# Optimization experiments

Measured on AMD Instinct MI355X. Metric: run time of the kernel, lower is better.

Reference implementation:

```python
import jax, jax.numpy as jnp
from jax import lax
import numpy as np

B, T, S, U, E, V = 64, 50, 50, 1024, 100, 30001


def setup_inputs() -> dict:
    key = jax.random.key(0)
    ks = jax.random.split(key, 12)
    sc = 0.02
    return {
        "tokens": jax.random.randint(ks[0], (B, T), 0, V, dtype=jnp.int32),
        "memory": jax.random.normal(ks[1], (B, S, U), jnp.float32),
        "h0": jax.random.normal(ks[2], (B, U), jnp.float32),
        "c0": jax.random.normal(ks[3], (B, U), jnp.float32),
        "emb": jax.random.normal(ks[4], (V, E), jnp.float32) * sc,
        "Wx": jax.random.normal(ks[5], (E + U, 4 * U), jnp.float32) * sc,
        "Uh": jax.random.normal(ks[6], (U, 4 * U), jnp.float32) * sc,
        "b": jnp.zeros((4 * U,), jnp.float32),
        "Wm": jax.random.normal(ks[7], (U, U), jnp.float32) * sc,
        "Wa": jax.random.normal(ks[8], (2 * U, U), jnp.float32) * sc,
        "Wo": jax.random.normal(ks[9], (U, V), jnp.float32) * sc,
        "bo": jnp.zeros((V,), jnp.float32),
    }


def reference(tokens, memory, h0, c0, emb, Wx, Uh, b, Wm, Wa, Wo, bo):
    # Luong memory layer: keys = memory @ Wm (Dense(units, use_bias=False))
    keys = jnp.einsum("bsu,uk->bsk", memory, Wm)  # [B,S,U]
    x_emb = emb[tokens]                            # [B,T,E] teacher-forced inputs

    def step(carry, x_t):
        h, c, attn = carry
        # AttentionWrapper cell input: concat(embedding, prev attention)
        z = jnp.concatenate([x_t, attn], axis=-1) @ Wx + h @ Uh + b  # [B,4U]
        i, f, g, o = jnp.split(z, 4, axis=-1)  # keras gate order i,f,c,o
        c_new = jax.nn.sigmoid(f) * c + jax.nn.sigmoid(i) * jnp.tanh(g)
        h_new = jax.nn.sigmoid(o) * jnp.tanh(c_new)
        # Luong score: query (h_new) dot processed memory keys
        score = jnp.einsum("bu,bsu->bs", h_new, keys)
        align = jax.nn.softmax(score, axis=-1)
        ctx = jnp.einsum("bs,bsu->bu", align, memory)
        # attention_layer: Dense(units, use_bias=False) on concat(cell_out, ctx)
        attn_new = jnp.concatenate([h_new, ctx], axis=-1) @ Wa
        logits = attn_new @ Wo + bo  # output_layer
        return (h_new, c_new, attn_new), logits

    init = (h0, c0, jnp.zeros_like(h0))
    _, logits = lax.scan(step, init, jnp.swapaxes(x_emb, 0, 1))  # [T,B,V]
    return jnp.transpose(logits, (1, 0, 2))  # [B,T,V]
```

## Files before the change

### kernel.cpp

```cpp
#include <hip/hip_runtime.h>
#include <math.h>

#define B_  64
#define T_  50
#define S_  50
#define U_  1024
#define E_  100
#define V_  30001
#define U4_ 4096
#define VP_ 30080
#define HCSTR_ 131136

typedef __bf16 bf16_t;
typedef bf16_t bf16x8 __attribute__((ext_vector_type(8)));
typedef float  f32x4  __attribute__((ext_vector_type(4)));
typedef unsigned long long u64_t;

__device__ __forceinline__ float2 scload8(const float* p) {
    u64_t v = __hip_atomic_load((const u64_t*)p, __ATOMIC_RELAXED,
                                __HIP_MEMORY_SCOPE_SYSTEM);
    union { u64_t u; float2 f; } c; c.u = v; return c.f;
}
__device__ __forceinline__ void scstore8(float* p, float x, float y) {
    union { u64_t u; float2 f; } c; c.f = make_float2(x, y);
    __hip_atomic_store((u64_t*)p, c.u, __ATOMIC_RELAXED,
                       __HIP_MEMORY_SCOPE_SYSTEM);
}
__device__ __forceinline__ unsigned scload_u(const unsigned* p) {
    return __hip_atomic_load(p, __ATOMIC_RELAXED, __HIP_MEMORY_SCOPE_SYSTEM);
}
__device__ __forceinline__ void scadd_u(unsigned* p) {
    __hip_atomic_fetch_add(p, 1u, __ATOMIC_RELAXED, __HIP_MEMORY_SCOPE_SYSTEM);
}
__device__ __forceinline__ void vm_drain() {
    asm volatile("s_waitcnt vmcnt(0)" ::: "memory");
}
__device__ __forceinline__ void cbar() { asm volatile("" ::: "memory"); }

__global__ void add_inplace(float* __restrict__ dst, const float* __restrict__ src, int n)
{
    int i = blockIdx.x * blockDim.x + threadIdx.x;
    if (i < n) dst[i] += src[i];
}

__global__ void gather_emb_pad(const int* __restrict__ tokens,
                               const float* __restrict__ emb,
                               float* __restrict__ xe)
{
    const int r = blockIdx.x;
    const int e = threadIdx.x;
    float v;
    if (e < E_)       v = emb[(size_t)tokens[r] * E_ + e];
    else if (e == E_) v = 1.f;
    else              v = 0.f;
    xe[(size_t)r * 128 + e] = v;
}

__global__ void pad_wx(const float* __restrict__ Wx,
                       const float* __restrict__ bvec,
                       float* __restrict__ dst)
{
    const int col = blockIdx.x * 256 + threadIdx.x;
    const int row = blockIdx.y;
    float v;
    if (row < E_)       v = Wx[(size_t)row * U4_ + col];
    else if (row == E_) v = bvec[col];
    else                v = 0.f;
    dst[(size_t)row * U4_ + col] = v;
}

__global__ __launch_bounds__(256) void transpose_wo(
    const float* __restrict__ wo, bf16_t* __restrict__ dst)
{
    __shared__ bf16_t tile[64][72];
    const int c0 = blockIdx.x * 64;
    const int k0 = blockIdx.y * 64;
    const int tx = threadIdx.x & 63, ty = threadIdx.x >> 6;

#pragma unroll
    for (int kk = ty; kk < 64; kk += 4) {
        const int col = c0 + tx;
        float v = (col < V_) ? wo[(size_t)(k0 + kk) * V_ + col] : 0.f;
        tile[kk][tx] = (bf16_t)v;
    }
    __syncthreads();
#pragma unroll
    for (int cc = ty; cc < 64; cc += 4)
        dst[(size_t)(c0 + cc) * 1024 + k0 + tx] = tile[tx][cc];
}

template <int OUT>
__global__ __launch_bounds__(256) void gemm_mfma_split(
    const float* __restrict__ A, int lda,
    const float* __restrict__ Bm, int ldb,
    float* __restrict__ C, int ldc, int K)
{
    __shared__ bf16_t As_h[128][40];
    __shared__ bf16_t As_l[128][40];
    __shared__ bf16_t Bs_h[128][40];
    __shared__ bf16_t Bs_l[128][40];

    const int n0  = blockIdx.x * 128;
    const int m0  = blockIdx.y * 128;
    const int tid = threadIdx.x;
    const int wave = tid >> 6, lane = tid & 63;
    const int wr = wave >> 1, wc = wave & 1;
    const int lr = lane & 15;
    const int lk = lane >> 4;

    f32x4 acc[4][4] = {};

    const int ar  = tid >> 1, ak = (tid & 1) * 16;
    const int bk0 = (tid >> 5) * 4, bc = (tid & 31) * 4;

    for (int k0 = 0; k0 < K; k0 += 32) {
        {
            const float* ap = &A[(size_t)(m0 + ar) * lda + k0 + ak];
            bf16x8 h0v, l0v, h1v, l1v;
#pragma unroll
            for (int q = 0; q < 2; ++q) {
                float4 v0 = *(const float4*)&ap[q * 8];
                float4 v1 = *(const float4*)&ap[q * 8 + 4];
                float xs[8] = {v0.x, v0.y, v0.z, v0.w, v1.x, v1.y, v1.z, v1.w};
#pragma unroll
                for (int e = 0; e < 8; ++e) {
                    bf16_t h = (bf16_t)xs[e];
                    if (q == 0) { h0v[e] = h; l0v[e] = (bf16_t)(xs[e] - (float)h); }
                    else        { h1v[e] = h; l1v[e] = (bf16_t)(xs[e] - (float)h); }
                }
            }
            *(bf16x8*)&As_h[ar][ak]     = h0v;
            *(bf16x8*)&As_h[ar][ak + 8] = h1v;
            *(bf16x8*)&As_l[ar][ak]     = l0v;
            *(bf16x8*)&As_l[ar][ak + 8] = l1v;
        }
        {
#pragma unroll
            for (int kk = 0; kk < 4; ++kk) {
                float4 v = *(const float4*)&Bm[(size_t)(k0 + bk0 + kk) * ldb + n0 + bc];
                float xs[4] = {v.x, v.y, v.z, v.w};
#pragma unroll
                for (int i = 0; i < 4; ++i) {
                    bf16_t h = (bf16_t)xs[i];
                    Bs_h[bc + i][bk0 + kk] = h;
                    Bs_l[bc + i][bk0 + kk] = (bf16_t)(xs[i] - (float)h);
                }
            }
        }
        __syncthreads();

        bf16x8 ah[4], alv[4], bh[4], bl[4];
#pragma unroll
        for (int m = 0; m < 4; ++m) {
            ah[m]  = *(const bf16x8*)&As_h[wr * 64 + m * 16 + lr][lk * 8];
            alv[m] = *(const bf16x8*)&As_l[wr * 64 + m * 16 + lr][lk * 8];
        }
#pragma unroll
        for (int n = 0; n < 4; ++n) {
            bh[n] = *(const bf16x8*)&Bs_h[wc * 64 + n * 16 + lr][lk * 8];
            bl[n] = *(const bf16x8*)&Bs_l[wc * 64 + n * 16 + lr][lk * 8];
        }
#pragma unroll
        for (int m = 0; m < 4; ++m)
#pragma unroll
            for (int n = 0; n < 4; ++n) {
                acc[m][n] = __builtin_amdgcn_mfma_f32_16x16x32_bf16(ah[m],  bh[n], acc[m][n], 0, 0, 0);
                acc[m][n] = __builtin_amdgcn_mfma_f32_16x16x32_bf16(ah[m],  bl[n], acc[m][n], 0, 0, 0);
                acc[m][n] = __builtin_amdgcn_mfma_f32_16x16x32_bf16(alv[m], bh[n], acc[m][n], 0, 0, 0);
            }
        __syncthreads();
    }

#pragma unroll
    for (int m = 0; m < 4; ++m) {
        const int row = m0 + wr * 64 + m * 16 + lk * 4;
#pragma unroll
        for (int n = 0; n < 4; ++n) {
            const int col = n0 + wc * 64 + n * 16 + lr;
#pragma unroll
            for (int r = 0; r < 4; ++r) {
                if (OUT == 0)
                    C[(size_t)(row + r) * ldc + col] = acc[m][n][r];
                else
                    ((bf16_t*)C)[(size_t)(row + r) * ldc + col] = (bf16_t)acc[m][n][r];
            }
        }
    }
}

__global__ __launch_bounds__(256) void zgemm_partial(
    const float* __restrict__ A, int lda,
    const float* __restrict__ Bm,
    float* __restrict__ zp)
{
    __shared__ float As[64][17];
    __shared__ float Bs[16][68];

    const int n0     = blockIdx.x * 64;
    const int ks     = blockIdx.y;
    const int k_base = ks * 256;
    const int tid    = threadIdx.x;
    const int tx     = tid & 15, ty = tid >> 4;

    float acc[4][4];
#pragma unroll
    for (int i = 0; i < 4; ++i)
#pragma unroll
        for (int j = 0; j < 4; ++j) acc[i][j] = 0.f;

    const int ra = tid >> 2, ca = (tid & 3) * 4;
    const int rb = tid >> 4, cb = (tid & 15) * 4;

    for (int kt = 0; kt < 16; ++kt) {
        const int k0 = k_base + kt * 16;
        float4 av = *(const float4*)&A[(size_t)ra * lda + k0 + ca];
        As[ra][ca + 0] = av.x;
        As[ra][ca + 1] = av.y;
        As[ra][ca + 2] = av.z;
        As[ra][ca + 3] = av.w;
        float4 bv = *(const float4*)&Bm[(size_t)(k0 + rb) * U4_ + n0 + cb];
        *(float4*)&Bs[rb][cb] = bv;
        __syncthreads();
#pragma unroll
        for (int kk = 0; kk < 16; ++kk) {
            float a_[4];
#pragma unroll
            for (int i = 0; i < 4; ++i) a_[i] = As[ty * 4 + i][kk];
            float4 bq = *(const float4*)&Bs[kk][tx * 4];
            float b_[4] = {bq.x, bq.y, bq.z, bq.w};
#pragma unroll
            for (int i = 0; i < 4; ++i)
#pragma unroll
                for (int j = 0; j < 4; ++j)
                    acc[i][j] = fmaf(a_[i], b_[j], acc[i][j]);
        }
        __syncthreads();
    }

#pragma unroll
    for (int i = 0; i < 4; ++i)
        *(float4*)&zp[((size_t)ks * 64 + ty * 4 + i) * U4_ + n0 + tx * 4] =
            make_float4(acc[i][0], acc[i][1], acc[i][2], acc[i][3]);
}

__global__ __launch_bounds__(512) void decoder_loop12(
    const float* __restrict__ zemb,
    const float* __restrict__ Wcomb,
    const float* __restrict__ keys,
    const float* __restrict__ memory,
    const float* __restrict__ c0,
    float* __restrict__ hcbuf,
    float* __restrict__ zp,
    float* __restrict__ hc_all,
    unsigned* flags)
{
    static __shared__ __attribute__((aligned(16))) char smem[153088];
    bf16_t* wfr = (bf16_t*)smem;
    float*  tr  = (float*)(smem + 131072);
    float*  hs  = (float*)(smem + 148480);
    float*  sc  = (float*)(smem + 152576);
    float*  al  = (float*)(smem + 152832);

    const int beta = blockIdx.x;
    const int tid  = threadIdx.x;

    const int nt = beta & 63, ks = beta >> 6;
    const int koff = ks * 512;
    const int c0c  = nt * 64;

    for (int i = tid; i < 512 * 64; i += 512) {
        const int k = i >> 6, col = i & 63;
        const float w = Wcomb[(size_t)(koff + k) * U4_ + c0c + col];
        const bf16_t hi = (bf16_t)w;
        const bf16_t lo = (bf16_t)(w - (float)hi);
        const int ntile = col >> 4, lane_lo = col & 15;
        const int kk = k >> 5, kr = k & 31;
        const int lane = (kr >> 3) * 16 + lane_lo, j = kr & 7;
        const int base = ((ntile * 16 + kk) * 2) * 512 + lane * 8 + j;
        wfr[base]       = hi;
        wfr[base + 512] = lo;
    }

    const int b  = beta;
    const int u2 = tid * 2;
    float creg[2] = {0.f, 0.f};
    if (beta < 64) {
        float2 cv = *(const float2*)&c0[b * U_ + u2];
        creg[0] = cv.x;
        creg[1] = cv.y;
    }
    __syncthreads();

    const int w  = tid >> 6, l = tid & 63;
    const int mt = w >> 1, ntb = (w & 1) * 2;
    const int arow = mt * 16 + (l & 15);
    const int aq   = l >> 4;
    const size_t abase = (size_t)arow * 2048 + koff + aq * 8;

    for (int t = 0; t < T_; ++t) {
        if (t) {
            {
                const unsigned tgt = 8u * (unsigned)t;
                const unsigned* fb = (ks < 2) ? &flags[512] : &flags[768];
                if (tid < 8) {
                    const unsigned* f = fb + tid * 32;
                    while (scload_u(f) < tgt) __builtin_amdgcn_s_sleep(1);
                }
                __syncthreads();
                cbar();
            }

            const float* ap = &hcbuf[(size_t)(t - 1) * HCSTR_ + abase];

            float4 a0[16], a1[16];
#pragma unroll
            for (int kk = 0; kk < 16; ++kk) {
                a0[kk] = *(const float4*)&ap[kk * 32];
                a1[kk] = *(const float4*)&ap[kk * 32 + 4];
            }

            f32x4 acc[2] = {};
#pragma unroll
            for (int kk = 0; kk < 16; ++kk) {
                float xs[8] = {a0[kk].x, a0[kk].y, a0[kk].z, a0[kk].w,
                               a1[kk].x, a1[kk].y, a1[kk].z, a1[kk].w};
                bf16x8 ah, alv;
#pragma unroll
                for (int e = 0; e < 8; ++e) {
                    bf16_t h = (bf16_t)xs[e];
                    ah[e]  = h;
                    alv[e] = (bf16_t)(xs[e] - (float)h);
                }
#pragma unroll
                for (int nn = 0; nn < 2; ++nn) {
                    const int fb2 = (((ntb + nn) * 16 + kk) * 2) * 512 + l * 8;
                    bf16x8 bh = *(const bf16x8*)&wfr[fb2];
                    bf16x8 bl = *(const bf16x8*)&wfr[fb2 + 512];
                    acc[nn] = __builtin_amdgcn_mfma_f32_16x16x32_bf16(ah, bh, acc[nn], 0, 0, 0);
                    acc[nn] = __builtin_amdgcn_mfma_f32_16x16x32_bf16(ah, bl, acc[nn], 0, 0, 0);
                    acc[nn] = __builtin_amdgcn_mfma_f32_16x16x32_bf16(alv, bh, acc[nn], 0, 0, 0);
                }
            }

#pragma unroll
            for (int nn = 0; nn < 2; ++nn)
#pragma unroll
                for (int rr = 0; rr < 4; ++rr)
                    tr[(mt * 16 + (l >> 4) * 4 + rr) * 68 + (ntb + nn) * 16 + (l & 15)] =
                        acc[nn][rr];
            __syncthreads();

            {
                const int zb = tid >> 3, cg = (tid & 7) * 8;
                float4 r0 = *(const float4*)&tr[zb * 68 + cg];
                float4 r1 = *(const float4*)&tr[zb * 68 + cg + 4];
                float* zrow = &zp[((size_t)(ks * 64 + zb)) * U4_ + c0c + cg];
                scstore8(zrow + 0, r0.x, r0.y);
                scstore8(zrow + 2, r0.z, r0.w);
                scstore8(zrow + 4, r1.x, r1.y);
                scstore8(zrow + 6, r1.z, r1.w);
            }
            vm_drain();
            __syncthreads();
            if (tid == 0) scadd_u(&flags[(beta & 15) * 32]);
        }

        if (beta < 64) {
            if (t) {
                const unsigned tgt = 16u * (unsigned)t;
                if (tid < 16) {
                    const unsigned* f = &flags[tid * 32];
                    while (scload_u(f) < tgt) __builtin_amdgcn_s_sleep(1);
                }
                __syncthreads();
                cbar();
            }

            const float* ze = &zemb[((size_t)b * T_ + t) * U4_];
            float zgx[4], zgy[4];
#pragma unroll
            for (int g = 0; g < 4; ++g) {
                float2 a = *(const float2*)&ze[g * U_ + u2];
                zgx[g] = a.x;
                zgy[g] = a.y;
            }
#pragma unroll
            for (int s = 0; s < 4; ++s) {
#pragma unroll
                for (int g = 0; g < 4; ++g) {
                    float2 v = scload8(&zp[((size_t)s * 64 + b) * U4_ + g * U_ + u2]);
                    zgx[g] += v.x;
                    zgy[g] += v.y;
                }
            }

            const float six = 1.f / (1.f + expf(-zgx[0]));
            const float sfx = 1.f / (1.f + expf(-zgx[1]));
            const float tgx = tanhf(zgx[2]);
            const float sox = 1.f / (1.f + expf(-zgx[3]));
            const float cnx = sfx * creg[0] + six * tgx;
            creg[0] = cnx;
            const float hnx = sox * tanhf(cnx);

            const float siy = 1.f / (1.f + expf(-zgy[0]));
            const float sfy = 1.f / (1.f + expf(-zgy[1]));
            const float tgy = tanhf(zgy[2]);
            const float soy = 1.f / (1.f + expf(-zgy[3]));
            const float cny = sfy * creg[1] + siy * tgy;
            creg[1] = cny;
            const float hny = soy * tanhf(cny);

            float* hcb_t = &hcbuf[(size_t)t * HCSTR_];
            hs[u2]     = hnx;
            hs[u2 + 1] = hny;
            scstore8(&hcb_t[b * 2048 + u2], hnx, hny);
            *(float2*)&hc_all[((size_t)b * T_ + t) * 2048 + u2] =
                make_float2(hnx, hny);
            vm_drain();
            __syncthreads();
            if (tid == 0) scadd_u(&flags[512 + (b & 7) * 32]);

            const int lane = tid & 63, wv = tid >> 6;
            for (int s = wv; s < S_; s += 8) {
                const float* kp = &keys[((size_t)b * S_ + s) * U_ + lane * 16];
                const float* hp = &hs[lane * 16];
                float p = 0.f;
#pragma unroll
                for (int q = 0; q < 4; ++q) {
                    float4 kv = *(const float4*)&kp[q * 4];
                    float4 hv = *(const float4*)&hp[q * 4];
                    p = fmaf(hv.x, kv.x, p);
                    p = fmaf(hv.y, kv.y, p);
                    p = fmaf(hv.z, kv.z, p);
                    p = fmaf(hv.w, kv.w, p);
                }
#pragma unroll
                for (int off = 32; off > 0; off >>= 1)
                    p += __shfl_xor(p, off);
                if (lane == 0) sc[s] = p;
            }
            __syncthreads();

            if (tid < 64) {
                float v = (tid < S_) ? sc[tid] : -INFINITY;
                float m = v;
#pragma unroll
                for (int off = 32; off > 0; off >>= 1)
                    m = fmaxf(m, __shfl_xor(m, off));
                float e = (tid < S_) ? expf(v - m) : 0.f;
                float ssum = e;
#pragma unroll
                for (int off = 32; off > 0; off >>= 1)
                    ssum += __shfl_xor(ssum, off);
                if (tid < S_) al[tid] = e / ssum;
            }
            __syncthreads();

            {
                const float2* mp = (const float2*)&memory[(size_t)b * S_ * U_];
                float cx = 0.f, cy = 0.f;
#pragma unroll 10
                for (int s = 0; s < S_; ++s) {
                    float2 mv = mp[s * 512 + tid];
                    const float a = al[s];
                    cx = fmaf(a, mv.x, cx);
                    cy = fmaf(a, mv.y, cy);
                }
                scstore8(&hcb_t[b * 2048 + U_ + u2], cx, cy);
                *(float2*)&hc_all[((size_t)b * T_ + t) * 2048 + U_ + u2] =
                    make_float2(cx, cy);
            }
            vm_drain();
            __syncthreads();
            if (tid == 0) scadd_u(&flags[768 + (b & 7) * 32]);
        }
    }
}

__global__ __launch_bounds__(256) void gemm_wo_mfma3(
    const bf16_t* __restrict__ A,
    const bf16_t* __restrict__ Bt,
    const float*  __restrict__ bias,
    float* __restrict__ C)
{
    __shared__ bf16_t As[2][128][40];
    __shared__ bf16_t Bs[2][128][40];

    const int n0  = blockIdx.x * 128;
    const int m0  = blockIdx.y * 128;
    const int tid = threadIdx.x;
    const int wave = tid >> 6, lane = tid & 63;
    const int wr = wave >> 1, wc = wave & 1;
    const int lr = lane & 15;
    const int lk = lane >> 4;

    f32x4 acc[4][4] = {};

    const int ar = tid >> 1, ak = (tid & 1) * 16;
    const bf16_t* apb = &A[(size_t)(m0 + ar) * U_ + ak];
    const bf16_t* bpb = &Bt[(size_t)(n0 + ar) * U_ + ak];

    {
        *(bf16x8*)&As[0][ar][ak]     = *(const bf16x8*)&apb[0];
        *(bf16x8*)&As[0][ar][ak + 8] = *(const bf16x8*)&apb[8];
        *(bf16x8*)&Bs[0][ar][ak]     = *(const bf16x8*)&bpb[0];
        *(bf16x8*)&Bs[0][ar][ak + 8] = *(const bf16x8*)&bpb[8];
    }
    __syncthreads();

    for (int k0 = 0; k0 < U_; k0 += 32) {
        const int cur = (k0 >> 5) & 1;
        bf16x8 na0, na1, nb0, nb1;
        const bool more = (k0 + 32 < U_);
        if (more) {
            na0 = *(const bf16x8*)&apb[k0 + 32];
            na1 = *(const bf16x8*)&apb[k0 + 40];
            nb0 = *(const bf16x8*)&bpb[k0 + 32];
            nb1 = *(const bf16x8*)&bpb[k0 + 40];
        }

        bf16x8 af[4], bf[4];
#pragma unroll
        for (int m = 0; m < 4; ++m)
            af[m] = *(const bf16x8*)&As[cur][wr * 64 + m * 16 + lr][lk * 8];
#pragma unroll
        for (int n = 0; n < 4; ++n)
            bf[n] = *(const bf16x8*)&Bs[cur][wc * 64 + n * 16 + lr][lk * 8];
#pragma unroll
        for (int m = 0; m < 4; ++m)
#pragma unroll
            for (int n = 0; n < 4; ++n)
                acc[m][n] = __builtin_amdgcn_mfma_f32_16x16x32_bf16(
                    af[m], bf[n], acc[m][n], 0, 0, 0);

        if (more) {
            *(bf16x8*)&As[cur ^ 1][ar][ak]     = na0;
            *(bf16x8*)&As[cur ^ 1][ar][ak + 8] = na1;
            *(bf16x8*)&Bs[cur ^ 1][ar][ak]     = nb0;
            *(bf16x8*)&Bs[cur ^ 1][ar][ak + 8] = nb1;
        }
        __syncthreads();
    }

#pragma unroll
    for (int m = 0; m < 4; ++m) {
        const int row = m0 + wr * 64 + m * 16 + lk * 4;
#pragma unroll
        for (int n = 0; n < 4; ++n) {
            const int col = n0 + wc * 64 + n * 16 + lr;
            if (col < V_) {
                const float bb = bias[col];
#pragma unroll
                for (int r = 0; r < 4; ++r)
                    C[(size_t)(row + r) * V_ + col] = acc[m][n][r] + bb;
            }
        }
    }
}

extern "C" void kernel_launch(void* const* d_in, const int* in_sizes, int n_in,
                              void* d_out, int out_size, void* d_ws, size_t ws_size,
                              hipStream_t stream)
{
    const int*   tokens = (const int*)  d_in[0];
    const float* memory = (const float*)d_in[1];
    const float* h0     = (const float*)d_in[2];
    const float* c0     = (const float*)d_in[3];
    const float* emb    = (const float*)d_in[4];
    const float* Wx     = (const float*)d_in[5];
    const float* Uh     = (const float*)d_in[6];
    const float* bvec   = (const float*)d_in[7];
    const float* Wm     = (const float*)d_in[8];
    const float* Wa     = (const float*)d_in[9];
    const float* Wo     = (const float*)d_in[10];
    const float* bo     = (const float*)d_in[11];
    float* out = (float*)d_out;

    float* ws = (float*)d_ws;
    size_t off = 0;
    float*   Wcomb  = ws + off; off += (size_t)2048 * U4_;
    float*   keys   = ws + off; off += (size_t)B_ * S_ * U_;
    float*   hc_all = ws + off; off += (size_t)B_ * T_ * 2048;
    float*   zp     = ws + off; off += (size_t)4 * B_ * U4_;
    float*   x_emb  = ws + off; off += (size_t)B_ * T_ * 128;
    unsigned* flags = (unsigned*)(ws + off); off += 1024;
    bf16_t*  wo_t   = (bf16_t*)(ws + off); off += (size_t)VP_ * 1024 / 2;

    float* zemb   = out;
    float* hcbuf  = out + (size_t)3200 * U4_;
    float* wx_pad = out + (size_t)3200 * U4_ + (size_t)T_ * HCSTR_;
    bf16_t* abf   = (bf16_t*)Wcomb;

    (void)ws_size;
    (void)hipMemsetAsync(flags, 0, 1024 * sizeof(unsigned), stream);

    gather_emb_pad<<<B_ * T_, 128, 0, stream>>>(tokens, emb, x_emb);
    pad_wx<<<dim3(U4_ / 256, 128), 256, 0, stream>>>(Wx, bvec, wx_pad);
    gemm_mfma_split<0><<<dim3(32, 25), 256, 0, stream>>>(
        x_emb, 128, wx_pad, U4_, zemb, U4_, 128);
    gemm_mfma_split<0><<<dim3(32, 16), 256, 0, stream>>>(
        Wa, U_, Wx + (size_t)E_ * U4_, U4_, Wcomb, U4_, U_);
    add_inplace<<<(1024 * U4_) / 256, 256, 0, stream>>>(Wcomb, Uh, 1024 * U4_);
    gemm_mfma_split<0><<<dim3(8, 25), 256, 0, stream>>>(
        memory, U_, Wm, U_, keys, U_, U_);
    zgemm_partial<<<dim3(64, 4), 256, 0, stream>>>(h0, U_, Uh, zp);
    transpose_wo<<<dim3(VP_ / 64, 1024 / 64), 256, 0, stream>>>(Wo, wo_t);

    decoder_loop12<<<256, 512, 0, stream>>>(
        zemb, Wcomb, keys, memory, c0, hcbuf, zp, hc_all, flags);

    gemm_mfma_split<1><<<dim3(8, 25), 256, 0, stream>>>(
        hc_all, 2048, Wa, U_, (float*)abf, U_, 2048);
    gemm_wo_mfma3<<<dim3(VP_ / 128, 25), 256, 0, stream>>>(abf, wo_t, bo, out);
}
```

Before: 2.147 ms.

## Precompute memory projected through the ctx rows of Wcomb to halve the recurrent GEMM K

Precomputes M2 = memory @ Wcomb[ctx rows] ahead of the loop. The context term of the gates then becomes an alignment-weighted sum over M2 inside the owning block, so the recurrent MFMA GEMM only needs h (K=1024 instead of 2048). This removes the context flag wait and the cross-block context exchange, and halves each block's LDS weight slice. The per-step context vectors for the output path are rebuilt afterwards by a separate ctx_recon kernel from the stored alignments. In exchange there is an extra large precompute GEMM, and each step streams 50x4096 floats of M2 per batch row, which is more global traffic on the serial critical path.

Result: slower. 2.672 ms (+24.4%).

```diff
diff --git a/kernel.cpp b/kernel.cpp
--- a/kernel.cpp
+++ b/kernel.cpp
@@ -9,22 +9,22 @@
 #define V_  30001
 #define U4_ 4096
 #define VP_ 30080
-#define HCSTR_ 131136
+#define HSTR_ 65600
 
 typedef __bf16 bf16_t;
 typedef bf16_t bf16x8 __attribute__((ext_vector_type(8)));
 typedef float  f32x4  __attribute__((ext_vector_type(4)));
 typedef unsigned long long u64_t;
 
+__device__ __forceinline__ void scstore8(float* p, float x, float y) {
+    union { u64_t u; float2 f; } c; c.f = make_float2(x, y);
+    __hip_atomic_store((u64_t*)p, c.u, __ATOMIC_RELAXED,
+                       __HIP_MEMORY_SCOPE_SYSTEM);
+}
 __device__ __forceinline__ float2 scload8(const float* p) {
     u64_t v = __hip_atomic_load((const u64_t*)p, __ATOMIC_RELAXED,
                                 __HIP_MEMORY_SCOPE_SYSTEM);
     union { u64_t u; float2 f; } c; c.u = v; return c.f;
-}
-__device__ __forceinline__ void scstore8(float* p, float x, float y) {
-    union { u64_t u; float2 f; } c; c.f = make_float2(x, y);
-    __hip_atomic_store((u64_t*)p, c.u, __ATOMIC_RELAXED,
-                       __HIP_MEMORY_SCOPE_SYSTEM);
 }
 __device__ __forceinline__ unsigned scload_u(const unsigned* p) {
     return __hip_atomic_load(p, __ATOMIC_RELAXED, __HIP_MEMORY_SCOPE_SYSTEM);
@@ -243,32 +243,65 @@
             make_float4(acc[i][0], acc[i][1], acc[i][2], acc[i][3]);
 }
 
-__global__ __launch_bounds__(512) void decoder_loop12(
+__global__ __launch_bounds__(512) void ctx_recon(
+    const float* __restrict__ align_all,
+    const float* __restrict__ memory,
+    float* __restrict__ hc_all)
+{
+    __shared__ float alds[T_ * 64];
+    const int b = blockIdx.x, tid = threadIdx.x;
+    for (int i = tid; i < T_ * 64; i += 512)
+        alds[i] = align_all[(size_t)b * T_ * 64 + i];
+    __syncthreads();
+    const int u2 = tid * 2;
+    for (int t0 = 0; t0 < T_; t0 += 10) {
+        float ax[10], ay[10];
+#pragma unroll
+        for (int q = 0; q < 10; ++q) { ax[q] = 0.f; ay[q] = 0.f; }
+        for (int s = 0; s < S_; ++s) {
+            float2 mv = *(const float2*)&memory[((size_t)b * S_ + s) * U_ + u2];
+#pragma unroll
+            for (int q = 0; q < 10; ++q) {
+                float a = alds[(t0 + q) * 64 + s];
+                ax[q] = fmaf(a, mv.x, ax[q]);
+                ay[q] = fmaf(a, mv.y, ay[q]);
+            }
+        }
+#pragma unroll
+        for (int q = 0; q < 10; ++q)
+            *(float2*)&hc_all[((size_t)b * T_ + t0 + q) * 2048 + U_ + u2] =
+                make_float2(ax[q], ay[q]);
+    }
+}
+
+__global__ __launch_bounds__(512) void decoder_loop13(
     const float* __restrict__ zemb,
     const float* __restrict__ Wcomb,
+    const float* __restrict__ M2,
     const float* __restrict__ keys,
     const float* __restrict__ memory,
     const float* __restrict__ c0,
-    float* __restrict__ hcbuf,
+    float* __restrict__ hbuf,
     float* __restrict__ zp,
     float* __restrict__ hc_all,
+    float* __restrict__ align_all,
     unsigned* flags)
 {
-    static __shared__ __attribute__((aligned(16))) char smem[153088];
+    static __shared__ __attribute__((aligned(16))) char smem[87552];
     bf16_t* wfr = (bf16_t*)smem;
-    float*  tr  = (float*)(smem + 131072);
-    float*  hs  = (float*)(smem + 148480);
-    float*  sc  = (float*)(smem + 152576);
-    float*  al  = (float*)(smem + 152832);
+    float*  tr  = (float*)(smem + 65536);
+    float*  hs  = (float*)(smem + 82944);
+    float*  sc  = (float*)(smem + 87040);
+    float*  al  = (float*)(smem + 87296);
 
     const int beta = blockIdx.x;
     const int tid  = threadIdx.x;
 
     const int nt = beta & 63, ks = beta >> 6;
-    const int koff = ks * 512;
+    const int koff = ks * 256;
     const int c0c  = nt * 64;
 
-    for (int i = tid; i < 512 * 64; i += 512) {
+    for (int i = tid; i < 256 * 64; i += 512) {
         const int k = i >> 6, col = i & 63;
         const float w = Wcomb[(size_t)(koff + k) * U4_ + c0c + col];
         const bf16_t hi = (bf16_t)w;
@@ -276,7 +309,7 @@
         const int ntile = col >> 4, lane_lo = col & 15;
         const int kk = k >> 5, kr = k & 31;
         const int lane = (kr >> 3) * 16 + lane_lo, j = kr & 7;
-        const int base = ((ntile * 16 + kk) * 2) * 512 + lane * 8 + j;
+        const int base = ((ntile * 8 + kk) * 2) * 512 + lane * 8 + j;
         wfr[base]       = hi;
         wfr[base + 512] = lo;
     }
@@ -284,6 +317,8 @@
     const int b  = beta;
     const int u2 = tid * 2;
     float creg[2] = {0.f, 0.f};
+    float zalx[4] = {0.f, 0.f, 0.f, 0.f};
+    float zaly[4] = {0.f, 0.f, 0.f, 0.f};
     if (beta < 64) {
         float2 cv = *(const float2*)&c0[b * U_ + u2];
         creg[0] = cv.x;
@@ -295,35 +330,28 @@
     const int mt = w >> 1, ntb = (w & 1) * 2;
     const int arow = mt * 16 + (l & 15);
     const int aq   = l >> 4;
-    const size_t abase = (size_t)arow * 2048 + koff + aq * 8;
+    const size_t abase = (size_t)arow * U_ + koff + aq * 8;
 
     for (int t = 0; t < T_; ++t) {
         if (t) {
             {
                 const unsigned tgt = 8u * (unsigned)t;
-                const unsigned* fb = (ks < 2) ? &flags[512] : &flags[768];
                 if (tid < 8) {
-                    const unsigned* f = fb + tid * 32;
+                    const unsigned* f = &flags[512 + tid * 32];
                     while (scload_u(f) < tgt) __builtin_amdgcn_s_sleep(1);
                 }
                 __syncthreads();
                 cbar();
             }
 
-            const float* ap = &hcbuf[(size_t)(t - 1) * HCSTR_ + abase];
-
-            float4 a0[16], a1[16];
-#pragma unroll
-            for (int kk = 0; kk < 16; ++kk) {
-                a0[kk] = *(const float4*)&ap[kk * 32];
-                a1[kk] = *(const float4*)&ap[kk * 32 + 4];
-            }
+            const float* ap = &hbuf[(size_t)(t - 1) * HSTR_ + abase];
 
             f32x4 acc[2] = {};
 #pragma unroll
-            for (int kk = 0; kk < 16; ++kk) {
-                float xs[8] = {a0[kk].x, a0[kk].y, a0[kk].z, a0[kk].w,
-                               a1[kk].x, a1[kk].y, a1[kk].z, a1[kk].w};
+            for (int kk = 0; kk < 8; ++kk) {
+                float4 a0 = *(const float4*)&ap[kk * 32];
+                float4 a1 = *(const float4*)&ap[kk * 32 + 4];
+                float xs[8] = {a0.x, a0.y, a0.z, a0.w, a1.x, a1.y, a1.z, a1.w};
                 bf16x8 ah, alv;
 #pragma unroll
                 for (int e = 0; e < 8; ++e) {
@@ -333,7 +361,7 @@
                 }
 #pragma unroll
                 for (int nn = 0; nn < 2; ++nn) {
-                    const int fb2 = (((ntb + nn) * 16 + kk) * 2) * 512 + l * 8;
+                    const int fb2 = (((ntb + nn) * 8 + kk) * 2) * 512 + l * 8;
                     bf16x8 bh = *(const bf16x8*)&wfr[fb2];
                     bf16x8 bl = *(const bf16x8*)&wfr[fb2 + 512];
                     acc[nn] = __builtin_amdgcn_mfma_f32_16x16x32_bf16(ah, bh, acc[nn], 0, 0, 0);
@@ -381,8 +409,8 @@
 #pragma unroll
             for (int g = 0; g < 4; ++g) {
                 float2 a = *(const float2*)&ze[g * U_ + u2];
-                zgx[g] = a.x;
-                zgy[g] = a.y;
+                zgx[g] = a.x + zalx[g];
+                zgy[g] = a.y + zaly[g];
             }
 #pragma unroll
             for (int s = 0; s < 4; ++s) {
@@ -410,10 +438,9 @@
             creg[1] = cny;
             const float hny = soy * tanhf(cny);
 
-            float* hcb_t = &hcbuf[(size_t)t * HCSTR_];
             hs[u2]     = hnx;
             hs[u2 + 1] = hny;
-            scstore8(&hcb_t[b * 2048 + u2], hnx, hny);
+            scstore8(&hbuf[(size_t)t * HSTR_ + b * U_ + u2], hnx, hny);
             *(float2*)&hc_all[((size_t)b * T_ + t) * 2048 + u2] =
                 make_float2(hnx, hny);
             vm_drain();
@@ -452,27 +479,26 @@
 #pragma unroll
                 for (int off = 32; off > 0; off >>= 1)
                     ssum += __shfl_xor(ssum, off);
-                if (tid < S_) al[tid] = e / ssum;
+                al[tid] = (tid < S_) ? e / ssum : 0.f;
             }
             __syncthreads();
 
-            {
-                const float2* mp = (const float2*)&memory[(size_t)b * S_ * U_];
-                float cx = 0.f, cy = 0.f;
-#pragma unroll 10
-                for (int s = 0; s < S_; ++s) {
-                    float2 mv = mp[s * 512 + tid];
-                    const float a = al[s];
-                    cx = fmaf(a, mv.x, cx);
-                    cy = fmaf(a, mv.y, cy);
-                }
-                scstore8(&hcb_t[b * 2048 + U_ + u2], cx, cy);
-                *(float2*)&hc_all[((size_t)b * T_ + t) * 2048 + U_ + u2] =
-                    make_float2(cx, cy);
-            }
-            vm_drain();
-            __syncthreads();
-            if (tid == 0) scadd_u(&flags[768 + (b & 7) * 32]);
+            if (tid < 64)
+                align_all[((size_t)b * T_ + t) * 64 + tid] = al[tid];
+
+#pragma unroll
+            for (int g = 0; g < 4; ++g) { zalx[g] = 0.f; zaly[g] = 0.f; }
+            const float* m2b = &M2[(size_t)b * S_ * U4_];
+            for (int s = 0; s < S_; ++s) {
+                const float a = al[s];
+                const float* mr = &m2b[(size_t)s * U4_];
+#pragma unroll
+                for (int g = 0; g < 4; ++g) {
+                    float2 mv = *(const float2*)&mr[g * U_ + u2];
+                    zalx[g] = fmaf(a, mv.x, zalx[g]);
+                    zaly[g] = fmaf(a, mv.y, zaly[g]);
+                }
+            }
         }
     }
 }
@@ -578,18 +604,20 @@
 
     float* ws = (float*)d_ws;
     size_t off = 0;
-    float*   Wcomb  = ws + off; off += (size_t)2048 * U4_;
-    float*   keys   = ws + off; off += (size_t)B_ * S_ * U_;
-    float*   hc_all = ws + off; off += (size_t)B_ * T_ * 2048;
-    float*   zp     = ws + off; off += (size_t)4 * B_ * U4_;
-    float*   x_emb  = ws + off; off += (size_t)B_ * T_ * 128;
-    unsigned* flags = (unsigned*)(ws + off); off += 1024;
-    bf16_t*  wo_t   = (bf16_t*)(ws + off); off += (size_t)VP_ * 1024 / 2;
+    float*   keys    = ws + off; off += (size_t)B_ * S_ * U_;
+    float*   hc_all  = ws + off; off += (size_t)B_ * T_ * 2048;
+    float*   zp      = ws + off; off += (size_t)4 * B_ * U4_;
+    float*   x_emb   = ws + off; off += (size_t)B_ * T_ * 128;
+    float*   al_all  = ws + off; off += (size_t)B_ * T_ * 64;
+    unsigned* flags  = (unsigned*)(ws + off); off += 1024;
+    bf16_t*  wo_t    = (bf16_t*)(ws + off); off += (size_t)VP_ * 1024 / 2;
 
     float* zemb   = out;
-    float* hcbuf  = out + (size_t)3200 * U4_;
-    float* wx_pad = out + (size_t)3200 * U4_ + (size_t)T_ * HCSTR_;
-    bf16_t* abf   = (bf16_t*)Wcomb;
+    float* hbuf   = zemb + (size_t)3200 * U4_;
+    float* wx_pad = hbuf + (size_t)T_ * HSTR_;
+    float* Wcomb  = wx_pad + (size_t)128 * U4_;
+    float* M2     = Wcomb + (size_t)2048 * U4_;
+    bf16_t* abf   = (bf16_t*)keys;
 
     (void)ws_size;
     (void)hipMemsetAsync(flags, 0, 1024 * sizeof(unsigned), stream);
@@ -601,14 +629,17 @@
     gemm_mfma_split<0><<<dim3(32, 16), 256, 0, stream>>>(
         Wa, U_, Wx + (size_t)E_ * U4_, U4_, Wcomb, U4_, U_);
     add_inplace<<<(1024 * U4_) / 256, 256, 0, stream>>>(Wcomb, Uh, 1024 * U4_);
+    gemm_mfma_split<0><<<dim3(32, 25), 256, 0, stream>>>(
+        memory, U_, Wcomb + (size_t)1024 * U4_, U4_, M2, U4_, U_);
     gemm_mfma_split<0><<<dim3(8, 25), 256, 0, stream>>>(
         memory, U_, Wm, U_, keys, U_, U_);
     zgemm_partial<<<dim3(64, 4), 256, 0, stream>>>(h0, U_, Uh, zp);
     transpose_wo<<<dim3(VP_ / 64, 1024 / 64), 256, 0, stream>>>(Wo, wo_t);
 
-    decoder_loop12<<<256, 512, 0, stream>>>(
-        zemb, Wcomb, keys, memory, c0, hcbuf, zp, hc_all, flags);
-
+    decoder_loop13<<<256, 512, 0, stream>>>(
+        zemb, Wcomb, M2, keys, memory, c0, hbuf, zp, hc_all, al_all, flags);
+
+    ctx_recon<<<B_, 512, 0, stream>>>(al_all, memory, hc_all);
     gemm_mfma_split<1><<<dim3(8, 25), 256, 0, stream>>>(
         hc_all, 2048, Wa, U_, (float*)abf, U_, 2048);
     gemm_wo_mfma3<<<dim3(VP_ / 128, 25), 256, 0, stream>>>(abf, wo_t, bo, out);
```
